# Kernel optimization log

Hardware: AMD Instinct MI355X
Metric: run time of the kernel (lower is better)

The kernel has to match this reference:

```python
import jax, jax.numpy as jnp
import numpy as np

HEADS = 4
ATTN_DIM = 32
SCALE = ATTN_DIM ** -0.5
EPS = 1e-12  # F.normalize eps


def rmsnorm_chan(x, g):
    # x: (b, c, h, w); RMSNorm over channel dim: F.normalize(x, dim=1) * g * sqrt(c)
    c = x.shape[1]
    n = jnp.sqrt(jnp.sum(x * x, axis=1, keepdims=True))
    return x / jnp.maximum(n, EPS) * g[None, :, None, None] * jnp.sqrt(jnp.asarray(c, x.dtype))


def setup_inputs() -> dict:
    key = jax.random.key(0)
    ks = jax.random.split(key, 4)
    b, c, h, w = 16, 256, 64, 64
    hidden = HEADS * ATTN_DIM  # 128
    x = jax.random.normal(ks[0], (b, c, h, w), dtype=jnp.float32)
    norm_g = jnp.ones((c,), jnp.float32)
    w_qkv = jax.random.normal(ks[1], (3 * hidden, c), dtype=jnp.float32) * 0.02
    mem_kv = jax.random.normal(ks[2], (2, HEADS, ATTN_DIM, 4), dtype=jnp.float32)
    w_out = jax.random.normal(ks[3], (c, hidden), dtype=jnp.float32) * 0.02
    b_out = jnp.zeros((c,), jnp.float32)
    out_norm_g = jnp.ones((c,), jnp.float32)
    return {"x": x, "norm_g": norm_g, "w_qkv": w_qkv, "mem_kv": mem_kv,
            "w_out": w_out, "b_out": b_out, "out_norm_g": out_norm_g}


def reference(x, norm_g, w_qkv, mem_kv, w_out, b_out, out_norm_g):
    b, c, h, w = x.shape
    n = h * w
    xn = rmsnorm_chan(x, norm_g).reshape(b, c, n)  # pre-norm, flatten spatial
    # 1x1 conv (no bias) == channel matmul: (b, 3*hidden, n)
    qkv = jnp.einsum('oc,bcn->bon', w_qkv, xn)
    q, k, v = jnp.split(qkv, 3, axis=1)
    # (b, heads, d, n)
    q = q.reshape(b, HEADS, ATTN_DIM, n)
    k = k.reshape(b, HEADS, ATTN_DIM, n)
    v = v.reshape(b, HEADS, ATTN_DIM, n)
    # prepend memory kv (broadcast over batch): (b, heads, d, num_mem + n)
    mk = jnp.broadcast_to(mem_kv[0][None], (b, HEADS, ATTN_DIM, mem_kv.shape[-1]))
    mv = jnp.broadcast_to(mem_kv[1][None], (b, HEADS, ATTN_DIM, mem_kv.shape[-1]))
    k = jnp.concatenate([mk, k], axis=-1)
    v = jnp.concatenate([mv, v], axis=-1)
    q = jax.nn.softmax(q, axis=-2) * SCALE  # softmax over feature dim d
    k = jax.nn.softmax(k, axis=-1)          # softmax over token dim n
    context = jnp.einsum('bhdn,bhen->bhde', k, v)   # small d x e per head
    out = jnp.einsum('bhde,bhdn->bhen', context, q)  # (b, heads, e, n)
    out = out.reshape(b, HEADS * ATTN_DIM, h, w)
    # 1x1 conv with bias, then RMSNorm
    out = jnp.einsum('oc,bchw->bohw', w_out, out) + b_out[None, :, None, None]
    return rmsnorm_chan(out, out_norm_g)
```

## Files before the change

### kernel.cpp

```cpp
#include <hip/hip_runtime.h>
#include <hip/hip_bf16.h>

typedef __hip_bfloat16 bf16;
typedef __attribute__((ext_vector_type(8))) short bf16x8;
typedef __attribute__((ext_vector_type(4))) float floatx4;

#define NB 16
#define NC 256
#define NPIX 4096
#define NHID 128
#define NH 4
#define ND 32
#define NMEM 4
#define QSCALE 0.17677669529663687f

#define VMCNT(n) asm volatile("s_waitcnt vmcnt(" #n ")" ::: "memory")
#define LGKM0()  asm volatile("s_waitcnt lgkmcnt(0)" ::: "memory")
#define SCHEDB() __builtin_amdgcn_sched_barrier(0)

__device__ __forceinline__ void dma16(const void* g, void* l){
  __builtin_amdgcn_global_load_lds(
      (const __attribute__((address_space(1))) unsigned int*)g,
      (__attribute__((address_space(3))) unsigned int*)l, 16, 0, 0);
}

__launch_bounds__(256)
__global__ void kW(const float* __restrict__ wqkv, const float* __restrict__ g,
                   bf16* __restrict__ wgpack, float* __restrict__ zbase){
  const int u = blockIdx.x*256 + threadIdx.x;
  for (int z = u; z < 65536 + 2048; z += 48*256) zbase[z] = 0.f;
  const int s = u / 1536;
  const int r = u - s*1536;
  const int tile = r >> 6, l = r & 63;
  const int row = tile*16 + (l & 15);
  const int kb  = s*32 + (l >> 4)*8;
  const float* wp = wqkv + (size_t)row*NC + kb;
  floatx4 w0 = *(const floatx4*)wp;
  floatx4 w1 = *(const floatx4*)(wp + 4);
  floatx4 g0 = *(const floatx4*)(g + kb);
  floatx4 g1 = *(const floatx4*)(g + kb + 4);
  alignas(16) bf16 tmp[8];
  #pragma unroll
  for (int i = 0; i < 4; ++i){
    tmp[i]   = __float2bfloat16(w0[i]*g0[i]);
    tmp[4+i] = __float2bfloat16(w1[i]*g1[i]);
  }
  *(uint4*)(wgpack + (size_t)u*8) = *(const uint4*)tmp;
}

__launch_bounds__(256)
__global__ void kA(const float* __restrict__ x, const bf16* __restrict__ wgpack,
                   float* __restrict__ dout,
                   float* __restrict__ ctxu, float* __restrict__ zacc){
  __shared__ char smem alignas(16) [60672];
  bf16 (*Pb)[72] = (bf16(*)[72])smem;
  bf16 (*Vb)[72] = (bf16(*)[72])(smem + 18432);
  float* ssqL = (float*)(smem + 59392);
  float* sL   = (float*)(smem + 60416);
  const int t = threadIdx.x;
  const int pb = blockIdx.x * 64, b = blockIdx.y;
  const int wv = t >> 6, lane = t & 63, m = lane & 15, q4 = lane >> 4;
  const int px_st = t & 63, cg_st = t >> 6;
  const float* xb = x + (size_t)b*NC*NPIX;
  float ssq = 0.f;
  float xr[2][8];

  auto xissue = [&](int c, float* dst){
    const float* xp = xb + (size_t)(c*32 + cg_st*8)*NPIX + pb + px_st;
    #pragma unroll
    for (int j = 0; j < 8; ++j) dst[j] = xp[(size_t)j*NPIX];
  };
  auto xwrite = [&](int c, const float* v){
    alignas(16) bf16 tmp[8];
    #pragma unroll
    for (int j = 0; j < 8; ++j){
      ssq += v[j]*v[j];
      tmp[j] = __float2bfloat16(v[j]);
    }
    bf16 (*Xb)[40] = (bf16(*)[40])(smem + 49152 + (c&1)*5120);
    *(uint4*)&Xb[px_st][cg_st*8] = *(const uint4*)tmp;
  };
  auto dmaw = [&](int c){
    const bf16* gt = wgpack + ((size_t)(c*24 + wv*6)*64 + lane)*8;
    char* lt = smem + (c&1)*24576 + wv*6144;
    #pragma unroll
    for (int tt = 0; tt < 6; ++tt) dma16(gt + tt*512, lt + tt*1024);
  };

  xissue(0, xr[0]);
  SCHEDB();
  dmaw(0);
  SCHEDB();
  xissue(1, xr[1]);
  SCHEDB();
  xwrite(0, xr[0]);
  LGKM0();
  VMCNT(8);
  __builtin_amdgcn_s_barrier();
  SCHEDB();

  floatx4 acc[6][4] = {};
  #pragma unroll
  for (int s = 0; s < 8; ++s){
    const int buf = s & 1;
    bf16 (*Xb)[40] = (bf16(*)[40])(smem + 49152 + buf*5120);
    const bf16* Ab = (const bf16*)(smem + buf*24576);
    bf16x8 bfr[4], af[6];
    #pragma unroll
    for (int pt = 0; pt < 4; ++pt)
      bfr[pt] = *(const bf16x8*)&Xb[pt*16 + m][q4*8];
    #pragma unroll
    for (int rt = 0; rt < 6; ++rt)
      af[rt] = *(const bf16x8*)(Ab + (size_t)wv*3072 + rt*512 + (q4*16 + m)*8);
    if (s < 7) dmaw(s + 1);
    SCHEDB();
    if (s < 6) xissue(s + 2, xr[buf]);
    SCHEDB();
    #pragma unroll
    for (int rt = 0; rt < 6; ++rt)
      #pragma unroll
      for (int pt = 0; pt < 4; ++pt)
        acc[rt][pt] = __builtin_amdgcn_mfma_f32_16x16x32_bf16(af[rt], bfr[pt], acc[rt][pt], 0, 0, 0);
    if (s < 7) xwrite(s + 1, xr[buf ^ 1]);
    LGKM0();
    if (s < 6) { VMCNT(8); } else { VMCNT(0); }
    __builtin_amdgcn_s_barrier();
    SCHEDB();
  }
  ssqL[cg_st*64 + px_st] = ssq;
  __syncthreads();
  if (t < 64){
    float tot = ssqL[t] + ssqL[64 + t] + ssqL[128 + t] + ssqL[192 + t];
    sL[t] = 16.0f / fmaxf(sqrtf(tot), 1e-12f);
  }
  __syncthreads();
  float sv[4];
  #pragma unroll
  for (int pt = 0; pt < 4; ++pt) sv[pt] = sL[pt*16 + m];
  #pragma unroll
  for (int pr = 0; pr < 3; ++pr){
    const int ra = 2*pr, rb = 2*pr + 1;
    const int row0 = wv*96 + pr*32;
    const int type = row0 >> 7;
    if (type == 0){
      const int slice = row0 >> 5;
      const int j0 = (q4 & 1)*4;
      #pragma unroll
      for (int pt = 0; pt < 4; ++pt){
        float va[4], vb[4];
        float mx = -1e30f;
        #pragma unroll
        for (int r = 0; r < 4; ++r){
          va[r] = acc[ra][pt][r]*sv[pt];
          vb[r] = acc[rb][pt][r]*sv[pt];
          mx = fmaxf(mx, fmaxf(va[r], vb[r]));
        }
        mx = fmaxf(mx, __shfl_xor(mx, 16, 64));
        mx = fmaxf(mx, __shfl_xor(mx, 32, 64));
        float se = 0.f;
        #pragma unroll
        for (int r = 0; r < 4; ++r){
          va[r] = __expf(va[r] - mx); vb[r] = __expf(vb[r] - mx);
          se += va[r] + vb[r];
        }
        se += __shfl_xor(se, 16, 64);
        se += __shfl_xor(se, 32, 64);
        const float inv = QSCALE / se;
        alignas(8) bf16 pka[4], pkb[4];
        #pragma unroll
        for (int r = 0; r < 4; ++r){
          pka[r] = __float2bfloat16(va[r]*inv);
          pkb[r] = __float2bfloat16(vb[r]*inv);
        }
        const int ca = (slice*4 + pt)*4 + (q4 >> 1);
        const int cb = ca + 2;
        bf16* pa = (bf16*)(dout + (size_t)(b*NC + ca)*NPIX + pb) + m*8 + j0;
        bf16* pv = (bf16*)(dout + (size_t)(b*NC + cb)*NPIX + pb) + m*8 + j0;
        *(uint2*)pa = *(const uint2*)pka;
        *(uint2*)pv = *(const uint2*)pkb;
      }
    } else if (type == 1){
      const int d0 = row0 - 128;
      float za[4] = {}, zb[4] = {};
      #pragma unroll
      for (int pt = 0; pt < 4; ++pt){
        #pragma unroll
        for (int r = 0; r < 4; ++r){
          float pa = __expf(acc[ra][pt][r]*sv[pt]);
          float pv = __expf(acc[rb][pt][r]*sv[pt]);
          za[r] += pa; zb[r] += pv;
          Pb[d0      + q4*4 + r][pt*16 + m] = __float2bfloat16(pa);
          Pb[d0 + 16 + q4*4 + r][pt*16 + m] = __float2bfloat16(pv);
        }
      }
      #pragma unroll
      for (int r = 0; r < 4; ++r){
        #pragma unroll
        for (int o = 1; o < 16; o <<= 1){
          za[r] += __shfl_xor(za[r], o, 64);
          zb[r] += __shfl_xor(zb[r], o, 64);
        }
      }
      if (m == 0){
        #pragma unroll
        for (int r = 0; r < 4; ++r){
          atomicAdd(&zacc[b*NHID + d0      + q4*4 + r], za[r]);
          atomicAdd(&zacc[b*NHID + d0 + 16 + q4*4 + r], zb[r]);
        }
      }
    } else {
      const int v0 = row0 - 256;
      #pragma unroll
      for (int pt = 0; pt < 4; ++pt)
        #pragma unroll
        for (int r = 0; r < 4; ++r){
          Vb[v0      + q4*4 + r][pt*16 + m] = __float2bfloat16(acc[ra][pt][r]*sv[pt]);
          Vb[v0 + 16 + q4*4 + r][pt*16 + m] = __float2bfloat16(acc[rb][pt][r]*sv[pt]);
        }
    }
  }
  __syncthreads();
  floatx4 cx[2][2] = {};
  #pragma unroll
  for (int k0t = 0; k0t < 64; k0t += 32){
    bf16x8 af2[2], bf2[2];
    #pragma unroll
    for (int dt = 0; dt < 2; ++dt) af2[dt] = *(const bf16x8*)&Pb[wv*32 + dt*16 + m][k0t + q4*8];
    #pragma unroll
    for (int et = 0; et < 2; ++et) bf2[et] = *(const bf16x8*)&Vb[wv*32 + et*16 + m][k0t + q4*8];
    #pragma unroll
    for (int dt = 0; dt < 2; ++dt)
      #pragma unroll
      for (int et = 0; et < 2; ++et)
        cx[dt][et] = __builtin_amdgcn_mfma_f32_16x16x32_bf16(af2[dt], bf2[et], cx[dt][et], 0, 0, 0);
  }
  float* cb2 = ctxu + (size_t)(b*NH + wv)*ND*ND;
  #pragma unroll
  for (int dt = 0; dt < 2; ++dt)
    #pragma unroll
    for (int et = 0; et < 2; ++et)
      #pragma unroll
      for (int r = 0; r < 4; ++r)
        atomicAdd(&cb2[(dt*16 + q4*4 + r)*ND + et*16 + m], cx[dt][et][r]);
}

__launch_bounds__(256)
__global__ void k4_weff(const float* __restrict__ ctxu, const float* __restrict__ zacc,
                        const float* __restrict__ memkv, const float* __restrict__ wout,
                        bf16* __restrict__ wpack){
  __shared__ float ctxL[4][32][32];
  __shared__ float woutL[64][129];
  const int t = threadIdx.x;
  const int o0 = blockIdx.x * 64, b = blockIdx.y;
  {
    const float* ws = wout + (size_t)o0*NHID;
    #pragma unroll
    for (int i = 0; i < 32; ++i){
      const int idx = i*256 + t;
      woutL[idx >> 7][idx & 127] = ws[idx];
    }
  }
  if (t < 128){
    const int h = t >> 5;
    const float* mk = memkv + t*NMEM;
    float me[4]; float z = zacc[b*NHID + t];
    #pragma unroll
    for (int j = 0; j < 4; ++j){ me[j] = __expf(mk[j]); z += me[j]; }
    const float invz = 1.0f / z;
    const float* cp = ctxu + (size_t)(b*NH*ND + t)*ND;
    const float* mv = memkv + (size_t)(NHID + h*ND)*NMEM;
    #pragma unroll
    for (int e = 0; e < ND; ++e){
      float ce = cp[e];
      #pragma unroll
      for (int j = 0; j < 4; ++j) ce += me[j]*mv[e*NMEM + j];
      ctxL[h][t & 31][e] = ce * invz;
    }
  }
  __syncthreads();
  const int ol = t & 63, g = t >> 6;
  float out[32] = {};
  #pragma unroll
  for (int e = 0; e < 32; ++e){
    const float we = woutL[ol][g*32 + e];
    #pragma unroll
    for (int d = 0; d < 32; ++d) out[d] += ctxL[g][d][e] * we;
  }
  const int o = o0 + ol, tile = o >> 4, m16 = o & 15;
  #pragma unroll
  for (int q4k = 0; q4k < 4; ++q4k){
    alignas(16) bf16 tmp[8];
    #pragma unroll
    for (int j = 0; j < 8; ++j) tmp[j] = __float2bfloat16(out[q4k*8 + j]);
    *(uint4*)(wpack + ((size_t)((b*4 + g)*16 + tile)*64 + q4k*16 + m16)*8) = *(const uint4*)tmp;
  }
}

__launch_bounds__(256)
__global__ void k5_out(float* dout, const bf16* __restrict__ wpack,
                       const float* __restrict__ bout, const float* __restrict__ gout){
  __shared__ char smem alignas(16) [50432];
  bf16* Qb = (bf16*)(smem + 32768);
  float* red = (float*)(smem + 49152);
  float* nf  = (float*)(smem + 50176);
  const int t = threadIdx.x;
  const int pb = blockIdx.x * 64, b = blockIdx.y;
  const int wv = t >> 6, lane = t & 63, m = lane & 15, q4 = lane >> 4;
  {
    #pragma unroll
    for (int i = 0; i < 4; ++i){
      const int tau = wv*4 + i;
      const char* gq = (const char*)(dout + (size_t)(b*NC + tau*4 + q4)*NPIX + pb) + m*16;
      dma16(gq, smem + 32768 + tau*1024);
    }
  }
  {
    const bf16* gt = wpack + ((size_t)((b*4)*16 + wv*4)*64 + lane)*8;
    char* lt = smem + wv*4096;
    #pragma unroll
    for (int tt = 0; tt < 4; ++tt) dma16(gt + tt*512, lt + tt*1024);
  }
  VMCNT(0);
  __builtin_amdgcn_s_barrier();
  SCHEDB();
  floatx4 acc[4][4] = {};
  #pragma unroll
  for (int s = 0; s < 4; ++s){
    const int buf = s & 1;
    const bf16* Wb = (const bf16*)(smem + buf*16384);
    bf16x8 bfr[4], af[4];
    #pragma unroll
    for (int pt = 0; pt < 4; ++pt)
      bfr[pt] = *(const bf16x8*)(Qb + (size_t)(s*4 + pt)*512 + (q4*16 + m)*8);
    #pragma unroll
    for (int rt = 0; rt < 4; ++rt)
      af[rt] = *(const bf16x8*)(Wb + (size_t)(wv*4 + rt)*512 + (q4*16 + m)*8);
    if (s < 3){
      const bf16* gt = wpack + ((size_t)((b*4 + s+1)*16 + wv*4)*64 + lane)*8;
      char* lt = smem + (buf^1)*16384 + wv*4096;
      #pragma unroll
      for (int tt = 0; tt < 4; ++tt) dma16(gt + tt*512, lt + tt*1024);
    }
    SCHEDB();
    #pragma unroll
    for (int rt = 0; rt < 4; ++rt)
      #pragma unroll
      for (int pt = 0; pt < 4; ++pt)
        acc[rt][pt] = __builtin_amdgcn_mfma_f32_16x16x32_bf16(af[rt], bfr[pt], acc[rt][pt], 0, 0, 0);
    if (s < 3) { VMCNT(0); }
    SCHEDB();
  }
  float ps[4] = {0.f, 0.f, 0.f, 0.f};
  #pragma unroll
  for (int rt = 0; rt < 4; ++rt){
    const int row = wv*64 + rt*16 + q4*4;
    #pragma unroll
    for (int r = 0; r < 4; ++r){
      const float bias = bout[row + r];
      #pragma unroll
      for (int pt = 0; pt < 4; ++pt){
        acc[rt][pt][r] += bias;
        ps[pt] += acc[rt][pt][r]*acc[rt][pt][r];
      }
    }
  }
  #pragma unroll
  for (int pt = 0; pt < 4; ++pt){
    ps[pt] += __shfl_xor(ps[pt], 16, 64);
    ps[pt] += __shfl_xor(ps[pt], 32, 64);
  }
  if (q4 == 0){
    #pragma unroll
    for (int pt = 0; pt < 4; ++pt) red[wv*64 + pt*16 + m] = ps[pt];
  }
  __syncthreads();
  if (t < 64){
    float tot = red[t] + red[64 + t] + red[128 + t] + red[192 + t];
    nf[t] = 16.0f / fmaxf(sqrtf(tot), 1e-12f);
  }
  __syncthreads();
  float nv[4];
  #pragma unroll
  for (int pt = 0; pt < 4; ++pt) nv[pt] = nf[pt*16 + m];
  #pragma unroll
  for (int rt = 0; rt < 4; ++rt){
    const int row = wv*64 + rt*16 + q4*4;
    #pragma unroll
    for (int r = 0; r < 4; ++r){
      const float gg = gout[row + r];
      float* op = dout + (size_t)(b*NC + row + r)*NPIX + pb + m;
      #pragma unroll
      for (int pt = 0; pt < 4; ++pt)
        op[pt*16] = acc[rt][pt][r]*nv[pt]*gg;
    }
  }
}

extern "C" void kernel_launch(void* const* d_in, const int* in_sizes, int n_in,
                              void* d_out, int out_size, void* d_ws, size_t ws_size,
                              hipStream_t stream) {
  (void)in_sizes; (void)n_in; (void)out_size; (void)ws_size;
  const float* x     = (const float*)d_in[0];
  const float* ng    = (const float*)d_in[1];
  const float* wqkv  = (const float*)d_in[2];
  const float* memkv = (const float*)d_in[3];
  const float* wout  = (const float*)d_in[4];
  const float* bout  = (const float*)d_in[5];
  const float* gout  = (const float*)d_in[6];
  float* dout = (float*)d_out;
  char* ws = (char*)d_ws;
  bf16*  wgpack = (bf16*)(ws);
  bf16*  wpack  = (bf16*)(ws + 196608);
  float* ctxu   = (float*)(ws + 1245184);
  float* zacc   = (float*)(ws + 1507328);

  kW     <<<dim3(48),      256, 0, stream>>>(wqkv, ng, wgpack, ctxu);
  kA     <<<dim3(64, 16),  256, 0, stream>>>(x, wgpack, dout, ctxu, zacc);
  k4_weff<<<dim3(4, 16),   256, 0, stream>>>(ctxu, zacc, memkv, wout, wpack);
  k5_out <<<dim3(64, 16),  256, 0, stream>>>(dout, wpack, bout, gout);
}
```

Baseline: 178.6 us.

## Load MFMA operands directly from global into registers instead of LDS DMA

In kA, the weight fragments are now loaded from global memory straight into double-buffered registers, replacing the global_load_lds DMA into shared memory. This drops the explicit vmcnt waits and scheduling barriers and shrinks the LDS footprint, which may allow higher occupancy. In k5_out, all weight and activation fragments are preloaded into registers before a single MFMA loop, removing the LDS staging and barriers. The trade-off is higher VGPR pressure and reliance on the compiler to schedule and overlap the global loads.

```diff
diff --git a/kernel.cpp b/kernel.cpp
--- a/kernel.cpp
+++ b/kernel.cpp
@@ -14,15 +14,7 @@
 #define NMEM 4
 #define QSCALE 0.17677669529663687f
 
-#define VMCNT(n) asm volatile("s_waitcnt vmcnt(" #n ")" ::: "memory")
 #define LGKM0()  asm volatile("s_waitcnt lgkmcnt(0)" ::: "memory")
-#define SCHEDB() __builtin_amdgcn_sched_barrier(0)
-
-__device__ __forceinline__ void dma16(const void* g, void* l){
-  __builtin_amdgcn_global_load_lds(
-      (const __attribute__((address_space(1))) unsigned int*)g,
-      (__attribute__((address_space(3))) unsigned int*)l, 16, 0, 0);
-}
 
 __launch_bounds__(256)
 __global__ void kW(const float* __restrict__ wqkv, const float* __restrict__ g,
@@ -52,11 +44,11 @@
 __global__ void kA(const float* __restrict__ x, const bf16* __restrict__ wgpack,
                    float* __restrict__ dout,
                    float* __restrict__ ctxu, float* __restrict__ zacc){
-  __shared__ char smem alignas(16) [60672];
+  __shared__ char smem alignas(16) [48384];
   bf16 (*Pb)[72] = (bf16(*)[72])smem;
   bf16 (*Vb)[72] = (bf16(*)[72])(smem + 18432);
-  float* ssqL = (float*)(smem + 59392);
-  float* sL   = (float*)(smem + 60416);
+  float* ssqL = (float*)(smem + 47104);
+  float* sL   = (float*)(smem + 48128);
   const int t = threadIdx.x;
   const int pb = blockIdx.x * 64, b = blockIdx.y;
   const int wv = t >> 6, lane = t & 63, m = lane & 15, q4 = lane >> 4;
@@ -64,6 +56,7 @@
   const float* xb = x + (size_t)b*NC*NPIX;
   float ssq = 0.f;
   float xr[2][8];
+  bf16x8 af[2][6];
 
   auto xissue = [&](int c, float* dst){
     const float* xp = xb + (size_t)(c*32 + cg_st*8)*NPIX + pb + px_st;
@@ -77,55 +70,43 @@
       ssq += v[j]*v[j];
       tmp[j] = __float2bfloat16(v[j]);
     }
-    bf16 (*Xb)[40] = (bf16(*)[40])(smem + 49152 + (c&1)*5120);
+    bf16 (*Xb)[40] = (bf16(*)[40])(smem + 36864 + (c&1)*5120);
     *(uint4*)&Xb[px_st][cg_st*8] = *(const uint4*)tmp;
   };
-  auto dmaw = [&](int c){
-    const bf16* gt = wgpack + ((size_t)(c*24 + wv*6)*64 + lane)*8;
-    char* lt = smem + (c&1)*24576 + wv*6144;
-    #pragma unroll
-    for (int tt = 0; tt < 6; ++tt) dma16(gt + tt*512, lt + tt*1024);
+  auto wload = [&](int c, int rt)->bf16x8 {
+    return *(const bf16x8*)(wgpack + ((size_t)(c*24 + wv*6 + rt)*64 + lane)*8);
   };
 
   xissue(0, xr[0]);
-  SCHEDB();
-  dmaw(0);
-  SCHEDB();
+  #pragma unroll
+  for (int rt = 0; rt < 6; ++rt) af[0][rt] = wload(0, rt);
   xissue(1, xr[1]);
-  SCHEDB();
   xwrite(0, xr[0]);
   LGKM0();
-  VMCNT(8);
   __builtin_amdgcn_s_barrier();
-  SCHEDB();
 
   floatx4 acc[6][4] = {};
   #pragma unroll
   for (int s = 0; s < 8; ++s){
     const int buf = s & 1;
-    bf16 (*Xb)[40] = (bf16(*)[40])(smem + 49152 + buf*5120);
-    const bf16* Ab = (const bf16*)(smem + buf*24576);
-    bf16x8 bfr[4], af[6];
+    bf16 (*Xb)[40] = (bf16(*)[40])(smem + 36864 + buf*5120);
+    bf16x8 bfr[4];
     #pragma unroll
     for (int pt = 0; pt < 4; ++pt)
       bfr[pt] = *(const bf16x8*)&Xb[pt*16 + m][q4*8];
+    if (s < 7){
+      #pragma unroll
+      for (int rt = 0; rt < 6; ++rt) af[(s+1)&1][rt] = wload(s + 1, rt);
+    }
+    if (s < 6) xissue(s + 2, xr[buf]);
     #pragma unroll
     for (int rt = 0; rt < 6; ++rt)
-      af[rt] = *(const bf16x8*)(Ab + (size_t)wv*3072 + rt*512 + (q4*16 + m)*8);
-    if (s < 7) dmaw(s + 1);
-    SCHEDB();
-    if (s < 6) xissue(s + 2, xr[buf]);
-    SCHEDB();
-    #pragma unroll
-    for (int rt = 0; rt < 6; ++rt)
       #pragma unroll
       for (int pt = 0; pt < 4; ++pt)
-        acc[rt][pt] = __builtin_amdgcn_mfma_f32_16x16x32_bf16(af[rt], bfr[pt], acc[rt][pt], 0, 0, 0);
+        acc[rt][pt] = __builtin_amdgcn_mfma_f32_16x16x32_bf16(af[buf][rt], bfr[pt], acc[rt][pt], 0, 0, 0);
     if (s < 7) xwrite(s + 1, xr[buf ^ 1]);
     LGKM0();
-    if (s < 6) { VMCNT(8); } else { VMCNT(0); }
     __builtin_amdgcn_s_barrier();
-    SCHEDB();
   }
   ssqL[cg_st*64 + px_st] = ssq;
   __syncthreads();
@@ -299,57 +280,29 @@
 __launch_bounds__(256)
 __global__ void k5_out(float* dout, const bf16* __restrict__ wpack,
                        const float* __restrict__ bout, const float* __restrict__ gout){
-  __shared__ char smem alignas(16) [50432];
-  bf16* Qb = (bf16*)(smem + 32768);
-  float* red = (float*)(smem + 49152);
-  float* nf  = (float*)(smem + 50176);
+  __shared__ float red[256];
+  __shared__ float nf[64];
   const int t = threadIdx.x;
   const int pb = blockIdx.x * 64, b = blockIdx.y;
   const int wv = t >> 6, lane = t & 63, m = lane & 15, q4 = lane >> 4;
-  {
-    #pragma unroll
-    for (int i = 0; i < 4; ++i){
-      const int tau = wv*4 + i;
-      const char* gq = (const char*)(dout + (size_t)(b*NC + tau*4 + q4)*NPIX + pb) + m*16;
-      dma16(gq, smem + 32768 + tau*1024);
-    }
-  }
-  {
-    const bf16* gt = wpack + ((size_t)((b*4)*16 + wv*4)*64 + lane)*8;
-    char* lt = smem + wv*4096;
-    #pragma unroll
-    for (int tt = 0; tt < 4; ++tt) dma16(gt + tt*512, lt + tt*1024);
-  }
-  VMCNT(0);
-  __builtin_amdgcn_s_barrier();
-  SCHEDB();
+  bf16x8 wf[4][4], qf[4][4];
+  #pragma unroll
+  for (int s = 0; s < 4; ++s){
+    #pragma unroll
+    for (int rt = 0; rt < 4; ++rt)
+      wf[s][rt] = *(const bf16x8*)(wpack + ((size_t)((b*4 + s)*16 + wv*4 + rt)*64 + lane)*8);
+    #pragma unroll
+    for (int pt = 0; pt < 4; ++pt)
+      qf[s][pt] = *(const bf16x8*)((const char*)(dout + (size_t)(b*NC + (s*4 + pt)*4 + q4)*NPIX + pb) + m*16);
+  }
   floatx4 acc[4][4] = {};
   #pragma unroll
-  for (int s = 0; s < 4; ++s){
-    const int buf = s & 1;
-    const bf16* Wb = (const bf16*)(smem + buf*16384);
-    bf16x8 bfr[4], af[4];
-    #pragma unroll
-    for (int pt = 0; pt < 4; ++pt)
-      bfr[pt] = *(const bf16x8*)(Qb + (size_t)(s*4 + pt)*512 + (q4*16 + m)*8);
+  for (int s = 0; s < 4; ++s)
     #pragma unroll
     for (int rt = 0; rt < 4; ++rt)
-      af[rt] = *(const bf16x8*)(Wb + (size_t)(wv*4 + rt)*512 + (q4*16 + m)*8);
-    if (s < 3){
-      const bf16* gt = wpack + ((size_t)((b*4 + s+1)*16 + wv*4)*64 + lane)*8;
-      char* lt = smem + (buf^1)*16384 + wv*4096;
-      #pragma unroll
-      for (int tt = 0; tt < 4; ++tt) dma16(gt + tt*512, lt + tt*1024);
-    }
-    SCHEDB();
-    #pragma unroll
-    for (int rt = 0; rt < 4; ++rt)
       #pragma unroll
       for (int pt = 0; pt < 4; ++pt)
-        acc[rt][pt] = __builtin_amdgcn_mfma_f32_16x16x32_bf16(af[rt], bfr[pt], acc[rt][pt], 0, 0, 0);
-    if (s < 3) { VMCNT(0); }
-    SCHEDB();
-  }
+        acc[rt][pt] = __builtin_amdgcn_mfma_f32_16x16x32_bf16(wf[s][rt], qf[s][pt], acc[rt][pt], 0, 0, 0);
   float ps[4] = {0.f, 0.f, 0.f, 0.f};
   #pragma unroll
   for (int rt = 0; rt < 4; ++rt){
```

Result: no change. 176.4 us (-1.2%).
